# Optimization experiments

Measured on AMD Instinct MI355X. Metric: run time of the kernel, lower is better.

The kernel has to match this reference:

```python
import jax, jax.numpy as jnp
import numpy as np

B = 4_000_000  # number of box pairs


def _make_boxes(k_xy, k_wh):
    # valid (x1, y1, x2, y2) boxes: corner + positive width/height
    xy = jax.random.uniform(k_xy, (B, 2), minval=0.0, maxval=100.0, dtype=jnp.float32)
    wh = jax.random.uniform(k_wh, (B, 2), minval=1.0, maxval=50.0, dtype=jnp.float32)
    return jnp.concatenate([xy, xy + wh], axis=-1)  # [B, 4]


def setup_inputs() -> dict:
    key = jax.random.key(0)
    k1, k2, k3, k4 = jax.random.split(key, 4)
    return {
        "output": _make_boxes(k1, k2),
        "target": _make_boxes(k3, k4),
    }


def reference(output, target):
    # Batched version of the per-sample Python loop:
    # mean over batch of (1 - IoU(output[i], target[i])) using torchvision
    # box_iou math on matched pairs (diagonal of the pairwise IoU matrix).
    def area(b):
        return (b[:, 2] - b[:, 0]) * (b[:, 3] - b[:, 1])  # [B]

    lt = jnp.maximum(output[:, :2], target[:, :2])  # intersection top-left  [B,2]
    rb = jnp.minimum(output[:, 2:], target[:, 2:])  # intersection bot-right [B,2]
    wh = jnp.clip(rb - lt, 0.0)                      # clamp(min=0)          [B,2]
    inter = wh[:, 0] * wh[:, 1]                      # [B]
    union = area(output) + area(target) - inter      # [B]
    iou = inter / union                              # [B]
    return jnp.mean(1.0 - iou)                       # scalar mean loss
```

## Files before the change

### kernel.cpp

```cpp
#include <hip/hip_runtime.h>


#define BLOCK 256
#define NBLOCKS 1024

__global__ __launch_bounds__(BLOCK) void miou_partial(
    const float4* __restrict__ boxA,
    const float4* __restrict__ boxB,
    float* __restrict__ partials,
    int n)
{
    int tid = blockIdx.x * BLOCK + threadIdx.x;
    int stride = gridDim.x * BLOCK;

    float acc = 0.0f;
    for (int i = tid; i < n; i += stride) {
        float4 a = boxA[i];
        float4 b = boxB[i];

        float lt_x = fmaxf(a.x, b.x);
        float lt_y = fmaxf(a.y, b.y);
        float rb_x = fminf(a.z, b.z);
        float rb_y = fminf(a.w, b.w);

        float w = fmaxf(rb_x - lt_x, 0.0f);
        float h = fmaxf(rb_y - lt_y, 0.0f);
        float inter = w * h;

        float areaA = (a.z - a.x) * (a.w - a.y);
        float areaB = (b.z - b.x) * (b.w - b.y);
        float uni = areaA + areaB - inter;

        acc += 1.0f - inter / uni;
    }

    #pragma unroll
    for (int off = 32; off > 0; off >>= 1)
        acc += __shfl_down(acc, off, 64);

    __shared__ float s[BLOCK / 64];
    int lane = threadIdx.x & 63;
    int wid  = threadIdx.x >> 6;
    if (lane == 0) s[wid] = acc;
    __syncthreads();

    if (threadIdx.x == 0) {
        float t = 0.0f;
        #pragma unroll
        for (int w2 = 0; w2 < BLOCK / 64; ++w2) t += s[w2];
        partials[blockIdx.x] = t;
    }
}

__global__ __launch_bounds__(BLOCK) void miou_final(
    const float* __restrict__ partials, int np,
    float* __restrict__ out, int n)
{
    double acc = 0.0;
    for (int i = threadIdx.x; i < np; i += BLOCK)
        acc += (double)partials[i];

    #pragma unroll
    for (int off = 32; off > 0; off >>= 1)
        acc += __shfl_down(acc, off, 64);

    __shared__ double s[BLOCK / 64];
    int lane = threadIdx.x & 63;
    int wid  = threadIdx.x >> 6;
    if (lane == 0) s[wid] = acc;
    __syncthreads();

    if (threadIdx.x == 0) {
        double t = 0.0;
        #pragma unroll
        for (int w2 = 0; w2 < BLOCK / 64; ++w2) t += s[w2];
        out[0] = (float)(t / (double)n);
    }
}

extern "C" void kernel_launch(void* const* d_in, const int* in_sizes, int n_in,
                              void* d_out, int out_size, void* d_ws, size_t ws_size,
                              hipStream_t stream) {
    const float4* boxA = (const float4*)d_in[0];
    const float4* boxB = (const float4*)d_in[1];
    int n = in_sizes[0] / 4;

    float* partials = (float*)d_ws;
    float* out = (float*)d_out;

    miou_partial<<<NBLOCKS, BLOCK, 0, stream>>>(boxA, boxB, partials, n);
    miou_final<<<1, BLOCK, 0, stream>>>(partials, NBLOCKS, out, n);
}
```

Measured before the change: 26.21 us.

## Fuse final reduction into partial kernel via last-block atomic counter

Merges the two-kernel reduction into one kernel: each block publishes its partial sum and bumps an atomic counter, and the last block to arrive sums all partials in double and writes the mean. This removes the second kernel launch and its dependency gap. In exchange it adds a memset of the counter before every launch, plus acquire/release atomics.

Measured after the change: 54.18 us. +106.7%, slower.

```diff
diff --git a/kernel.cpp b/kernel.cpp
--- a/kernel.cpp
+++ b/kernel.cpp
@@ -4,10 +4,12 @@
 #define BLOCK 256
 #define NBLOCKS 1024
 
-__global__ __launch_bounds__(BLOCK) void miou_partial(
+__global__ __launch_bounds__(BLOCK) void miou_fused(
     const float4* __restrict__ boxA,
     const float4* __restrict__ boxB,
     float* __restrict__ partials,
+    unsigned* __restrict__ counter,
+    float* __restrict__ out,
     int n)
 {
     int tid = blockIdx.x * BLOCK + threadIdx.x;
@@ -39,42 +41,43 @@
         acc += __shfl_down(acc, off, 64);
 
     __shared__ float s[BLOCK / 64];
+    __shared__ bool isLast;
     int lane = threadIdx.x & 63;
     int wid  = threadIdx.x >> 6;
     if (lane == 0) s[wid] = acc;
     __syncthreads();
 
     if (threadIdx.x == 0) {
-        float t = 0.0f;
-        #pragma unroll
-        for (int w2 = 0; w2 < BLOCK / 64; ++w2) t += s[w2];
-        partials[blockIdx.x] = t;
+        float t = s[0] + s[1] + s[2] + s[3];
+        __hip_atomic_store(&partials[blockIdx.x], t,
+                           __ATOMIC_RELAXED, __HIP_MEMORY_SCOPE_AGENT);
+        unsigned old = __hip_atomic_fetch_add(counter, 1u,
+                           __ATOMIC_ACQ_REL, __HIP_MEMORY_SCOPE_AGENT);
+        isLast = (old == (unsigned)(NBLOCKS - 1));
     }
-}
-
-__global__ __launch_bounds__(BLOCK) void miou_final(
-    const float* __restrict__ partials, int np,
-    float* __restrict__ out, int n)
-{
-    double acc = 0.0;
-    for (int i = threadIdx.x; i < np; i += BLOCK)
-        acc += (double)partials[i];
-
-    #pragma unroll
-    for (int off = 32; off > 0; off >>= 1)
-        acc += __shfl_down(acc, off, 64);
-
-    __shared__ double s[BLOCK / 64];
-    int lane = threadIdx.x & 63;
-    int wid  = threadIdx.x >> 6;
-    if (lane == 0) s[wid] = acc;
     __syncthreads();
 
-    if (threadIdx.x == 0) {
-        double t = 0.0;
+    if (isLast) {
+        double dacc = 0.0;
         #pragma unroll
-        for (int w2 = 0; w2 < BLOCK / 64; ++w2) t += s[w2];
-        out[0] = (float)(t / (double)n);
+        for (int j = 0; j < NBLOCKS / BLOCK; ++j) {
+            float p = __hip_atomic_load(&partials[threadIdx.x + j * BLOCK],
+                          __ATOMIC_RELAXED, __HIP_MEMORY_SCOPE_AGENT);
+            dacc += (double)p;
+        }
+
+        #pragma unroll
+        for (int off = 32; off > 0; off >>= 1)
+            dacc += __shfl_down(dacc, off, 64);
+
+        __shared__ double sd[BLOCK / 64];
+        if (lane == 0) sd[wid] = dacc;
+        __syncthreads();
+
+        if (threadIdx.x == 0) {
+            double t = sd[0] + sd[1] + sd[2] + sd[3];
+            out[0] = (float)(t / (double)n);
+        }
     }
 }
 
@@ -85,9 +88,12 @@
     const float4* boxB = (const float4*)d_in[1];
     int n = in_sizes[0] / 4;
 
-    float* partials = (float*)d_ws;
-    float* out = (float*)d_out;
+    float*    partials = (float*)d_ws;
+    unsigned* counter  = (unsigned*)((char*)d_ws + NBLOCKS * 4);
+    float*    out      = (float*)d_out;
 
-    miou_partial<<<NBLOCKS, BLOCK, 0, stream>>>(boxA, boxB, partials, n);
-    miou_final<<<1, BLOCK, 0, stream>>>(partials, NBLOCKS, out, n);
+    hipMemsetAsync(counter, 0, sizeof(unsigned), stream);
+
+    miou_fused<<<NBLOCKS, BLOCK, 0, stream>>>(boxA, boxB, partials, counter,
+                                              out, n);
 }
```
